# Kernel tuning notes

Measured on AMD Instinct MI355X. Metric: run time of the kernel, lower is better.

The kernel has to match this reference:

```python
import jax, jax.numpy as jnp
import numpy as np

B, S, D, H = 2, 2048, 1024, 16
HD = D // H


def _linear_params(key, scale):
    kw, kb = jax.random.split(key)
    W = jax.random.normal(kw, (D, D), dtype=jnp.float32) * scale
    b = jax.random.normal(kb, (D,), dtype=jnp.float32) * scale
    return W, b


def setup_inputs() -> dict:
    key = jax.random.key(0)
    keys = jax.random.split(key, 10)
    scale = 1.0 / np.sqrt(D)
    vis = jax.random.normal(keys[0], (B, S, D), dtype=jnp.float32)
    inf = jax.random.normal(keys[1], (B, S, D), dtype=jnp.float32)
    names = ["q_vis", "k_vis", "v_vis", "q_inf", "k_inf", "v_inf", "o_vis", "o_inf"]
    out = {"vis": vis, "inf": inf}
    for n, k in zip(names, keys[2:]):
        W, b = _linear_params(k, scale)
        out["W_" + n] = W
        out["b_" + n] = b
    return out


def _heads(x):
    # [B,S,D] -> [B,H,S,HD]
    return x.reshape(B, S, H, HD).transpose(0, 2, 1, 3)


def _merge(x):
    # [B,H,S,HD] -> [B,S,D]
    return x.transpose(0, 2, 1, 3).reshape(B, S, D)


def reference(vis, inf, W_q_vis, b_q_vis, W_k_vis, b_k_vis, W_v_vis, b_v_vis,
              W_q_inf, b_q_inf, W_k_inf, b_k_inf, W_v_inf, b_v_inf,
              W_o_vis, b_o_vis, W_o_inf, b_o_inf):
    Qv = _heads(vis @ W_q_vis + b_q_vis)
    Kv = _heads(vis @ W_k_vis + b_k_vis)
    Vv = _heads(vis @ W_v_vis + b_v_vis)
    Qi = _heads(inf @ W_q_inf + b_q_inf)
    Ki = _heads(inf @ W_k_inf + b_k_inf)
    Vi = _heads(inf @ W_v_inf + b_v_inf)
    scale = 1.0 / jnp.sqrt(jnp.float32(HD))
    # vis queries attend over inf keys/values
    scores_vi = jnp.einsum("bhqd,bhkd->bhqk", Qv, Ki) * scale
    attn_inf = jax.nn.softmax(scores_vi, axis=-1)
    out_inf = jnp.einsum("bhqk,bhkd->bhqd", attn_inf, Vi)
    # inf queries attend over vis keys/values
    scores_iv = jnp.einsum("bhqd,bhkd->bhqk", Qi, Kv) * scale
    attn_vis = jax.nn.softmax(scores_iv, axis=-1)
    out_vis = jnp.einsum("bhqk,bhkd->bhqd", attn_vis, Vv)
    out_vis = _merge(out_vis) @ W_o_vis + b_o_vis
    out_inf = _merge(out_inf) @ W_o_inf + b_o_inf
    return (out_vis, out_inf)
```

## Files before the change

### kernel.cpp

```cpp
#include <hip/hip_runtime.h>
#include <hip/hip_bf16.h>

#define DEV __device__ __forceinline__

typedef __attribute__((ext_vector_type(4))) float f32x4;
typedef __attribute__((ext_vector_type(16))) float f32x16;
typedef __attribute__((ext_vector_type(8))) __bf16 bf16x8;
typedef __attribute__((ext_vector_type(8))) unsigned short ushort8;
typedef __attribute__((ext_vector_type(4))) unsigned int uint32x4;

static constexpr int BATCH = 2, SEQ = 2048, DM = 1024, NH = 16, HDIM = 64;
static constexpr size_t XSZ = (size_t)BATCH * SEQ * DM;

DEV unsigned short f2bf(float f) {
  union { float f; unsigned int u; } v; v.f = f;
  unsigned int r = (v.u + 0x7fffu + ((v.u >> 16) & 1u)) >> 16;
  return (unsigned short)r;
}

DEV bf16x8 ld8(const unsigned short* p) {
  return __builtin_bit_cast(bf16x8, *(const ushort8*)p);
}

DEV f32x4 mfma16(bf16x8 a, bf16x8 b, f32x4 c) {
  return __builtin_amdgcn_mfma_f32_16x16x32_bf16(a, b, c, 0, 0, 0);
}
DEV f32x16 mfma32(bf16x8 a, bf16x8 b, f32x16 c) {
  return __builtin_amdgcn_mfma_f32_32x32x16_bf16(a, b, c, 0, 0, 0);
}

DEV unsigned cvtpk(float lo, float hi) {
  unsigned r;
  asm("v_cvt_pk_bf16_f32 %0, %1, %2" : "=v"(r) : "v"(lo), "v"(hi));
  return r;
}
DEV void plswap(unsigned& a, unsigned& b) {
  asm("v_permlane32_swap_b32 %0, %1" : "+v"(a), "+v"(b));
}

DEV void gll16(const unsigned short* g, unsigned short* l) {
  __builtin_amdgcn_global_load_lds(
      (__attribute__((address_space(1))) void*)(unsigned short*)g,
      (__attribute__((address_space(3))) void*)l, 16, 0, 0);
}

__global__ __launch_bounds__(256)
void k_convert_x(const float* __restrict__ vis, const float* __restrict__ inff,
                 unsigned short* __restrict__ out) {
  const float* src = blockIdx.z ? inff : vis;
  unsigned short* dst = out + (size_t)blockIdx.z * XSZ;
  const size_t i = ((size_t)blockIdx.x * 256 + threadIdx.x) * 8;
  const float4 a = *(const float4*)(src + i);
  const float4 b = *(const float4*)(src + i + 4);
  ushort8 v;
  v[0] = f2bf(a.x); v[1] = f2bf(a.y); v[2] = f2bf(a.z); v[3] = f2bf(a.w);
  v[4] = f2bf(b.x); v[5] = f2bf(b.y); v[6] = f2bf(b.z); v[7] = f2bf(b.w);
  *(ushort8*)(dst + i) = v;
}

struct WPtrs { const float* w[8]; };

__global__ __launch_bounds__(256)
void k_convert_w(WPtrs p, unsigned short* __restrict__ wt) {
  const float* W = p.w[blockIdx.z];
  unsigned short* Wt = wt + (size_t)blockIdx.z * (1024 * 1024);
  const int k0 = blockIdx.y * 64, n0 = blockIdx.x * 64;
  __shared__ unsigned short t[64][68];
  const int tx = threadIdx.x & 15, ty = threadIdx.x >> 4;
#pragma unroll
  for (int i = 0; i < 4; ++i) {
    const int kr = ty * 4 + i;
    const float4 v = *(const float4*)(W + (size_t)(k0 + kr) * 1024 + n0 + tx * 4);
    t[kr][tx * 4 + 0] = f2bf(v.x); t[kr][tx * 4 + 1] = f2bf(v.y);
    t[kr][tx * 4 + 2] = f2bf(v.z); t[kr][tx * 4 + 3] = f2bf(v.w);
  }
  __syncthreads();
#pragma unroll
  for (int i = 0; i < 4; ++i) {
    const int nr = ty * 4 + i;
    ushort4 o;
    o.x = t[tx * 4 + 0][nr]; o.y = t[tx * 4 + 1][nr];
    o.z = t[tx * 4 + 2][nr]; o.w = t[tx * 4 + 3][nr];
    *(ushort4*)(Wt + (size_t)(n0 + nr) * 1024 + k0 + tx * 4) = o;
  }
}

struct GemmJob { const unsigned short* A; const unsigned short* W;
                 const float* bias; void* out; float scale; int mode; };
struct GemmJobs { GemmJob j[6]; };

__global__ __launch_bounds__(256)
void k_gemm(GemmJobs jobs) {
  const GemmJob jb = jobs.j[blockIdx.z];
  const int lane = threadIdx.x & 63, w = threadIdx.x >> 6;
  const int wr = w >> 1, wc = w & 1;
  const int r = lane & 15, g = lane >> 4;

  const int nid = blockIdx.x + (blockIdx.y << 3);
  const int bxs = nid >> 5;
  const int bys = ((nid & 7) << 2) + ((nid >> 3) & 3);
  const int bm = bys * 128, bn = bxs * 128;

  __shared__ __align__(16) unsigned short As[128 * 64];
  __shared__ __align__(16) unsigned short Bs[128 * 64];

  const int srow = lane >> 3;
  const int schunk = (lane & 7) ^ srow;
  const unsigned short* Ag = jb.A + (size_t)(bm + w * 32 + srow) * DM + schunk * 8;
  const unsigned short* Bg = jb.W + (size_t)(bn + w * 32 + srow) * DM + schunk * 8;

  f32x4 acc[4][4] = {};

  for (int kt = 0; kt < DM; kt += 64) {
#pragma unroll
    for (int j = 0; j < 4; ++j) {
      gll16(Ag + kt + j * 8 * DM, As + (w * 4 + j) * 512);
      gll16(Bg + kt + j * 8 * DM, Bs + (w * 4 + j) * 512);
    }
    __syncthreads();
#pragma unroll
    for (int kk = 0; kk < 2; ++kk) {
      bf16x8 a[4], b[4];
#pragma unroll
      for (int m = 0; m < 4; ++m) {
        const int row = wr * 64 + m * 16 + r;
        const int pos = (kk * 4 + g) ^ (row & 7);
        a[m] = ld8(As + row * 64 + pos * 8);
      }
#pragma unroll
      for (int n = 0; n < 4; ++n) {
        const int row = wc * 64 + n * 16 + r;
        const int pos = (kk * 4 + g) ^ (row & 7);
        b[n] = ld8(Bs + row * 64 + pos * 8);
      }
#pragma unroll
      for (int m = 0; m < 4; ++m)
#pragma unroll
        for (int n = 0; n < 4; ++n)
          acc[m][n] = mfma16(a[m], b[n], acc[m][n]);
    }
    __syncthreads();
  }

  if (jb.mode == 0) {
    unsigned short* O = (unsigned short*)jb.out;
#pragma unroll
    for (int n = 0; n < 4; ++n) {
      const int nc = bn + wc * 64 + n * 16 + r;
      const float bv = jb.bias[nc];
      const int h = nc >> 6, hd = nc & 63;
#pragma unroll
      for (int m = 0; m < 4; ++m)
#pragma unroll
        for (int i = 0; i < 4; ++i) {
          const int mr = bm + wr * 64 + m * 16 + g * 4 + i;
          const int bb = mr >> 11, s = mr & 2047;
          O[((size_t)(bb * NH + h) * SEQ + s) * HDIM + hd] =
              f2bf((acc[m][n][i] + bv) * jb.scale);
        }
    }
  } else if (jb.mode == 2) {
    unsigned short* O = (unsigned short*)jb.out;
#pragma unroll
    for (int n = 0; n < 4; ++n) {
      const int nc = bn + wc * 64 + n * 16 + r;
      const float bv = jb.bias[nc];
      const int h = nc >> 6, hd = nc & 63;
#pragma unroll
      for (int m = 0; m < 4; ++m) {
        const int mr = bm + wr * 64 + m * 16 + g * 4;
        const int bb = mr >> 11, s = mr & 2047;
        ushort4 pv;
        pv.x = f2bf(acc[m][n][0] + bv);
        pv.y = f2bf(acc[m][n][1] + bv);
        pv.z = f2bf(acc[m][n][2] + bv);
        pv.w = f2bf(acc[m][n][3] + bv);
        *(ushort4*)(O + ((size_t)(bb * NH + h) * HDIM + hd) * SEQ + s) = pv;
      }
    }
  } else {
    float* O = (float*)jb.out;
#pragma unroll
    for (int n = 0; n < 4; ++n) {
      const int nc = bn + wc * 64 + n * 16 + r;
      const float bv = jb.bias[nc];
#pragma unroll
      for (int m = 0; m < 4; ++m)
#pragma unroll
        for (int i = 0; i < 4; ++i) {
          const int mr = bm + wr * 64 + m * 16 + g * 4 + i;
          O[(size_t)mr * DM + nc] = acc[m][n][i] + bv;
        }
    }
  }
}

struct AttnJob { const unsigned short* Q; const unsigned short* K;
                 const unsigned short* Vt; unsigned short* O; };
struct AttnJobs { AttnJob j[2]; };

__global__ __launch_bounds__(256)
void k_attn(AttnJobs jobs) {
  const AttnJob jb = jobs.j[blockIdx.z];
  const int nid = blockIdx.x + (blockIdx.y << 4);
  const int bx = nid >> 5;
  const int bh = ((nid & 7) << 2) + ((nid >> 3) & 3);
  const int lane = threadIdx.x & 63, w = threadIdx.x >> 6;
  const int q5 = lane & 31, hi = lane >> 5;
  const int qrow = bx * 128 + w * 32 + q5;

  const unsigned short* Qp = jb.Q + (size_t)bh * SEQ * HDIM;
  const unsigned short* Kp = jb.K + (size_t)bh * SEQ * HDIM;
  const unsigned short* Vp = jb.Vt + (size_t)bh * HDIM * SEQ;

  __shared__ __align__(16) unsigned short Ks[3][64 * 64];
  __shared__ __align__(16) unsigned short Vs[3][64 * 64];

  bf16x8 qf[4];
#pragma unroll
  for (int c = 0; c < 4; ++c)
    qf[c] = ld8(Qp + (size_t)qrow * HDIM + c * 16 + hi * 8);

  ushort8 ov;
#pragma unroll
  for (int i = 0; i < 8; ++i) ov[i] = 0x3f80;
  const bf16x8 onesb = __builtin_bit_cast(bf16x8, ov);

  const int srow = lane >> 3;
  const int sslot = lane & 7;

  auto stage = [&](int buf, int kv0) {
#pragma unroll
    for (int j = 0; j < 2; ++j) {
      const int row = j * 32 + w * 8 + srow;
      const int u = sslot ^ (row & 7);
      gll16(Kp + (size_t)(kv0 + row) * HDIM + u * 8, Ks[buf] + (j * 32 + w * 8) * 64);
      gll16(Vp + (size_t)row * SEQ + kv0 + u * 8,    Vs[buf] + (j * 32 + w * 8) * 64);
    }
  };

  f32x16 o0 = {}, o1 = {}, lsum = {};
  float mrow = -1e30f;
  const int swz = q5 & 7;
  constexpr int NT = SEQ / 64;

  stage(0, 0);
  stage(1, 64);
  asm volatile("s_waitcnt vmcnt(4)" ::: "memory");
  __builtin_amdgcn_s_barrier();
  __builtin_amdgcn_sched_barrier(0);

  int cur = 0, sb = 2;
  for (int t = 0; t < NT; ++t) {
    if (t + 2 < NT) stage(sb, (t + 2) * 64);

    f32x16 s0 = {}, s1 = {};
    __builtin_amdgcn_s_setprio(1);
#pragma unroll
    for (int c = 0; c < 4; ++c) {
      const int sl = ((2 * c + hi) ^ swz) * 8;
      s0 = mfma32(ld8(Ks[cur] + q5 * 64 + sl), qf[c], s0);
      s1 = mfma32(ld8(Ks[cur] + (32 + q5) * 64 + sl), qf[c], s1);
    }
    __builtin_amdgcn_s_setprio(0);

    float tm[8];
#pragma unroll
    for (int r = 0; r < 8; ++r)
      tm[r] = fmaxf(fmaxf(s0[r], s0[r + 8]), fmaxf(s1[r], s1[r + 8]));
    float mx = fmaxf(fmaxf(fmaxf(tm[0], tm[1]), tm[2]),
                     fmaxf(fmaxf(tm[3], tm[4]), fmaxf(fmaxf(tm[5], tm[6]), tm[7])));
    mx = fmaxf(mx, __shfl_xor(mx, 32, 64));

    if (!__all(mx <= mrow + 11.5416f)) {
      const float mn = fmaxf(mx, mrow);
      const float al = __builtin_amdgcn_exp2f(mrow - mn);
      mrow = mn;
      lsum[0] *= al;
#pragma unroll
      for (int r = 0; r < 16; ++r) { o0[r] *= al; o1[r] *= al; }
    }

#pragma unroll
    for (int r = 0; r < 16; ++r) {
      s0[r] = __builtin_amdgcn_exp2f(s0[r] - mrow);
      s1[r] = __builtin_amdgcn_exp2f(s1[r] - mrow);
    }

    unsigned pk0[8], pk1[8];
#pragma unroll
    for (int ww = 0; ww < 8; ++ww) {
      pk0[ww] = cvtpk(s0[2 * ww], s0[2 * ww + 1]);
      pk1[ww] = cvtpk(s1[2 * ww], s1[2 * ww + 1]);
    }

    __builtin_amdgcn_s_setprio(1);
#pragma unroll
    for (int c = 0; c < 4; ++c) {
      const int wb = 4 * (c & 1);
      unsigned a0 = (c < 2) ? pk0[wb + 0] : pk1[wb + 0];
      unsigned a1 = (c < 2) ? pk0[wb + 1] : pk1[wb + 1];
      unsigned b0 = (c < 2) ? pk0[wb + 2] : pk1[wb + 2];
      unsigned b1 = (c < 2) ? pk0[wb + 3] : pk1[wb + 3];
      plswap(a0, b0);
      plswap(a1, b1);
      uint32x4 fw = {a0, a1, b0, b1};
      const bf16x8 pf = __builtin_bit_cast(bf16x8, fw);
      const int sl = ((2 * c + hi) ^ swz) * 8;
      o0 = mfma32(ld8(Vs[cur] + q5 * 64 + sl), pf, o0);
      o1 = mfma32(ld8(Vs[cur] + (32 + q5) * 64 + sl), pf, o1);
      lsum = mfma32(onesb, pf, lsum);
    }
    __builtin_amdgcn_s_setprio(0);

    if (t + 1 < NT) {
      if (t + 2 < NT) {
        asm volatile("s_waitcnt vmcnt(4)" ::: "memory");
      } else {
        asm volatile("s_waitcnt vmcnt(0)" ::: "memory");
      }
      __builtin_amdgcn_s_barrier();
      __builtin_amdgcn_sched_barrier(0);
    }
    sb = cur;
    cur = (cur == 2) ? 0 : cur + 1;
  }

  const float inv = 1.f / lsum[0];
  const int bb = bh >> 4, h = bh & 15;
  unsigned short* Ob = jb.O + ((size_t)bb * SEQ + qrow) * DM + h * HDIM;

  auto storeO = [&](const f32x16 oo, int dbase) {
#pragma unroll
    for (int g4 = 0; g4 < 4; ++g4) {
      ushort4 pv;
      pv.x = f2bf(oo[4 * g4 + 0] * inv);
      pv.y = f2bf(oo[4 * g4 + 1] * inv);
      pv.z = f2bf(oo[4 * g4 + 2] * inv);
      pv.w = f2bf(oo[4 * g4 + 3] * inv);
      *(ushort4*)(Ob + dbase + 8 * g4 + 4 * hi) = pv;
    }
  };
  storeO(o0, 0);
  storeO(o1, 32);
}

extern "C" void kernel_launch(void* const* d_in, const int* in_sizes, int n_in,
                              void* d_out, int out_size, void* d_ws, size_t ws_size,
                              hipStream_t stream) {
  const float* vis = (const float*)d_in[0];
  const float* inff = (const float*)d_in[1];

  unsigned short* xbf  = (unsigned short*)d_ws;
  unsigned short* wt   = xbf + 2 * XSZ;
  unsigned short* Qv   = wt + (size_t)8 * 1024 * 1024;
  unsigned short* Kv   = Qv + XSZ;
  unsigned short* Vv   = Kv + XSZ;
  unsigned short* Qi   = Vv + XSZ;
  unsigned short* Ki   = Qi + XSZ;
  unsigned short* Vi   = Ki + XSZ;
  unsigned short* Vvt  = Vi + XSZ;
  unsigned short* Vit  = Vvt + XSZ;
  unsigned short* atA  = Vit + XSZ;
  unsigned short* atB  = atA + XSZ;

  k_convert_x<<<dim3(2048, 1, 2), 256, 0, stream>>>(vis, inff, xbf);

  WPtrs wp;
  wp.w[0] = (const float*)d_in[2];  wp.w[1] = (const float*)d_in[4];
  wp.w[2] = (const float*)d_in[6];  wp.w[3] = (const float*)d_in[8];
  wp.w[4] = (const float*)d_in[10]; wp.w[5] = (const float*)d_in[12];
  wp.w[6] = (const float*)d_in[14]; wp.w[7] = (const float*)d_in[16];
  k_convert_w<<<dim3(16, 16, 8), 256, 0, stream>>>(wp, wt);

  const size_t WSZ = (size_t)1024 * 1024;
  const float qsc = 0.18033688011f;
  GemmJobs pj;
  pj.j[0] = { xbf,       wt + 0 * WSZ, (const float*)d_in[3],  (void*)Qv,  qsc, 0 };
  pj.j[1] = { xbf,       wt + 1 * WSZ, (const float*)d_in[5],  (void*)Kv,  1.f, 0 };
  pj.j[2] = { xbf,       wt + 2 * WSZ, (const float*)d_in[7],  (void*)Vvt, 1.f, 2 };
  pj.j[3] = { xbf + XSZ, wt + 3 * WSZ, (const float*)d_in[9],  (void*)Qi,  qsc, 0 };
  pj.j[4] = { xbf + XSZ, wt + 4 * WSZ, (const float*)d_in[11], (void*)Ki,  1.f, 0 };
  pj.j[5] = { xbf + XSZ, wt + 5 * WSZ, (const float*)d_in[13], (void*)Vit, 1.f, 2 };
  k_gemm<<<dim3(8, 32, 6), 256, 0, stream>>>(pj);

  AttnJobs aj;
  aj.j[0] = { Qv, Ki, Vit, atA };
  aj.j[1] = { Qi, Kv, Vvt, atB };
  k_attn<<<dim3(16, 32, 2), 256, 0, stream>>>(aj);

  GemmJobs oj;
  oj.j[0] = { atB, wt + 6 * WSZ, (const float*)d_in[15], d_out, 1.f, 1 };
  oj.j[1] = { atA, wt + 7 * WSZ, (const float*)d_in[17], (void*)((float*)d_out + XSZ), 1.f, 1 };
  for (int z = 2; z < 6; ++z) oj.j[z] = oj.j[0];
  k_gemm<<<dim3(8, 32, 2), 256, 0, stream>>>(oj);
}
```

Before: 313.8 us.

## Use 512-thread attention blocks and replace ones-MFMA row sum with VALU sum

Doubles the attention block to 8 waves covering 256 query rows, so each staged K/V tile in shared memory is reused by twice as many queries. The grid is halved and each thread issues one K and one V async load per stage, with the wait counts adjusted to match. The row-sum MFMA against a ones vector is replaced by accumulating exponentials in a scalar, combined across the two half-waves with a shuffle at the end. This trades extra VALU adds and a bigger block (with tighter launch bounds and register pressure) for fewer MFMAs and less global K/V traffic.

```diff
diff --git a/kernel.cpp b/kernel.cpp
--- a/kernel.cpp
+++ b/kernel.cpp
@@ -199,15 +199,15 @@
                  const unsigned short* Vt; unsigned short* O; };
 struct AttnJobs { AttnJob j[2]; };
 
-__global__ __launch_bounds__(256)
+__global__ __launch_bounds__(512, 4)
 void k_attn(AttnJobs jobs) {
   const AttnJob jb = jobs.j[blockIdx.z];
-  const int nid = blockIdx.x + (blockIdx.y << 4);
-  const int bx = nid >> 5;
+  const int nid = blockIdx.x + (blockIdx.y << 3);
+  const int qt = nid >> 5;
   const int bh = ((nid & 7) << 2) + ((nid >> 3) & 3);
   const int lane = threadIdx.x & 63, w = threadIdx.x >> 6;
   const int q5 = lane & 31, hi = lane >> 5;
-  const int qrow = bx * 128 + w * 32 + q5;
+  const int qrow = qt * 256 + w * 32 + q5;
 
   const unsigned short* Qp = jb.Q + (size_t)bh * SEQ * HDIM;
   const unsigned short* Kp = jb.K + (size_t)bh * SEQ * HDIM;
@@ -221,32 +221,24 @@
   for (int c = 0; c < 4; ++c)
     qf[c] = ld8(Qp + (size_t)qrow * HDIM + c * 16 + hi * 8);
 
-  ushort8 ov;
-#pragma unroll
-  for (int i = 0; i < 8; ++i) ov[i] = 0x3f80;
-  const bf16x8 onesb = __builtin_bit_cast(bf16x8, ov);
-
-  const int srow = lane >> 3;
-  const int sslot = lane & 7;
+  const int srow = w * 8 + (lane >> 3);
+  const int schunk = (lane & 7) ^ (srow & 7);
+  const unsigned short* Kg = Kp + (size_t)srow * HDIM + schunk * 8;
+  const unsigned short* Vg = Vp + (size_t)srow * SEQ + schunk * 8;
 
   auto stage = [&](int buf, int kv0) {
-#pragma unroll
-    for (int j = 0; j < 2; ++j) {
-      const int row = j * 32 + w * 8 + srow;
-      const int u = sslot ^ (row & 7);
-      gll16(Kp + (size_t)(kv0 + row) * HDIM + u * 8, Ks[buf] + (j * 32 + w * 8) * 64);
-      gll16(Vp + (size_t)row * SEQ + kv0 + u * 8,    Vs[buf] + (j * 32 + w * 8) * 64);
-    }
+    gll16(Kg + (size_t)kv0 * HDIM, Ks[buf] + w * 512);
+    gll16(Vg + kv0,                Vs[buf] + w * 512);
   };
 
-  f32x16 o0 = {}, o1 = {}, lsum = {};
-  float mrow = -1e30f;
+  f32x16 o0 = {}, o1 = {};
+  float mrow = -1e30f, lrow = 0.f;
   const int swz = q5 & 7;
   constexpr int NT = SEQ / 64;
 
   stage(0, 0);
   stage(1, 64);
-  asm volatile("s_waitcnt vmcnt(4)" ::: "memory");
+  asm volatile("s_waitcnt vmcnt(2)" ::: "memory");
   __builtin_amdgcn_s_barrier();
   __builtin_amdgcn_sched_barrier(0);
 
@@ -276,16 +268,18 @@
       const float mn = fmaxf(mx, mrow);
       const float al = __builtin_amdgcn_exp2f(mrow - mn);
       mrow = mn;
-      lsum[0] *= al;
+      lrow *= al;
 #pragma unroll
       for (int r = 0; r < 16; ++r) { o0[r] *= al; o1[r] *= al; }
     }
 
+    float ps0 = 0.f, ps1 = 0.f;
 #pragma unroll
     for (int r = 0; r < 16; ++r) {
-      s0[r] = __builtin_amdgcn_exp2f(s0[r] - mrow);
-      s1[r] = __builtin_amdgcn_exp2f(s1[r] - mrow);
-    }
+      s0[r] = __builtin_amdgcn_exp2f(s0[r] - mrow); ps0 += s0[r];
+      s1[r] = __builtin_amdgcn_exp2f(s1[r] - mrow); ps1 += s1[r];
+    }
+    lrow += ps0 + ps1;
 
     unsigned pk0[8], pk1[8];
 #pragma unroll
@@ -309,13 +303,12 @@
       const int sl = ((2 * c + hi) ^ swz) * 8;
       o0 = mfma32(ld8(Vs[cur] + q5 * 64 + sl), pf, o0);
       o1 = mfma32(ld8(Vs[cur] + (32 + q5) * 64 + sl), pf, o1);
-      lsum = mfma32(onesb, pf, lsum);
     }
     __builtin_amdgcn_s_setprio(0);
 
     if (t + 1 < NT) {
       if (t + 2 < NT) {
-        asm volatile("s_waitcnt vmcnt(4)" ::: "memory");
+        asm volatile("s_waitcnt vmcnt(2)" ::: "memory");
       } else {
         asm volatile("s_waitcnt vmcnt(0)" ::: "memory");
       }
@@ -326,7 +319,8 @@
     cur = (cur == 2) ? 0 : cur + 1;
   }
 
-  const float inv = 1.f / lsum[0];
+  const float ltot = lrow + __shfl_xor(lrow, 32, 64);
+  const float inv = 1.f / ltot;
   const int bb = bh >> 4, h = bh & 15;
   unsigned short* Ob = jb.O + ((size_t)bb * SEQ + qrow) * DM + h * HDIM;
 
@@ -387,7 +381,7 @@
   AttnJobs aj;
   aj.j[0] = { Qv, Ki, Vit, atA };
   aj.j[1] = { Qi, Kv, Vvt, atB };
-  k_attn<<<dim3(16, 32, 2), 256, 0, stream>>>(aj);
+  k_attn<<<dim3(8, 32, 2), 512, 0, stream>>>(aj);
 
   GemmJobs oj;
   oj.j[0] = { atB, wt + 6 * WSZ, (const float*)d_in[15], d_out, 1.f, 1 };
```

After: 303.8 us. 1.03x faster.
